# Kernel optimization log

Measured on AMD Instinct MI355X. Metric: run time of the kernel, lower is better.

The kernel has to match this reference:

```python
import jax, jax.numpy as jnp
import numpy as np

B, NQ, NK, H = 4, 2048, 2048, 512
TEMP = 1.0


def setup_inputs() -> dict:
    key = jax.random.key(0)
    ks = jax.random.split(key, 13)
    s = 0.02
    inp = {
        "query_feat": jax.random.normal(ks[0], (B, NQ, H), jnp.float32),
        "key_feat": jax.random.normal(ks[1], (B, NK, H), jnp.float32),
        "qm_uncert": jax.random.normal(ks[2], (B, NQ), jnp.float32),
        "md_uncert": jax.random.normal(ks[3], (B, NK), jnp.float32),
        "Wq": jax.random.normal(ks[4], (H, H), jnp.float32) * s,
        "bq": jnp.zeros((H,), jnp.float32),
        "Wk": jax.random.normal(ks[5], (H, H), jnp.float32) * s,
        "bk": jnp.zeros((H,), jnp.float32),
        "Wv": jax.random.normal(ks[6], (H, H), jnp.float32) * s,
        "bv": jnp.zeros((H,), jnp.float32),
        "Wo": jax.random.normal(ks[7], (H, H), jnp.float32) * s,
        "bo": jnp.zeros((H,), jnp.float32),
        "tau": jnp.float32(1.0),
    }
    return inp


def reference(query_feat, key_feat, qm_uncert, md_uncert,
              Wq, bq, Wk, bk, Wv, bv, Wo, bo, tau):
    h = query_feat.shape[-1]
    Q = query_feat @ Wq.T + bq          # [B,Nq,H]
    K = key_feat @ Wk.T + bk            # [B,Nk,H]
    V = key_feat @ Wv.T + bv            # [B,Nk,H]

    # scaled dot-product logits
    logits = jnp.einsum('bqh,bkh->bqk', Q, K) / jnp.sqrt(jnp.asarray(h, logits_dtype(Q)))

    # uncertainty weight: sigmoid(tau * (qm_i + md_j)), then sanitize (mult mode)
    u = jax.nn.sigmoid(tau * (qm_uncert[:, :, None] + md_uncert[:, None, :]))
    u = jnp.nan_to_num(u, nan=1.0, posinf=1e6, neginf=1e-6)
    u = jnp.clip(u, 1e-6, 1e6)
    row_sum = jnp.sum(jnp.abs(u), axis=-1, keepdims=True)
    u = jnp.where(row_sum <= 1e-12, jnp.asarray(1e-6, u.dtype), u)

    logits = (logits * u) / TEMP

    # rows fully masked to -1e9 get zeroed (no mask here, but kept for faithfulness)
    all_masked = jnp.all(logits == -1e9, axis=-1, keepdims=True)
    logits = jnp.where(all_masked, jnp.zeros_like(logits), logits)

    attn = jax.nn.softmax(logits, axis=-1)  # dropout p=0 -> identity
    att = jnp.einsum('bqk,bkh->bqh', attn, V)
    out = att @ Wo.T + bo
    return out, attn


def logits_dtype(x):
    return x.dtype
```

## Files before the change

### kernel.cpp

```cpp
#include <hip/hip_runtime.h>
#include <stdint.h>

#define DEVI static __device__ __forceinline__

typedef unsigned short u16;
typedef short bf16x8 __attribute__((ext_vector_type(8)));
typedef u16 u16x8 __attribute__((ext_vector_type(8)));
typedef u16 u16x4 __attribute__((ext_vector_type(4)));
typedef float f32x4 __attribute__((ext_vector_type(4)));

DEVI u16 f2bf(float f) {
    uint32_t u = __builtin_bit_cast(uint32_t, f);
    u += 0x7FFFu + ((u >> 16) & 1u);
    return (u16)(u >> 16);
}
DEVI float bf2f(u16 u) { return __builtin_bit_cast(float, (uint32_t)u << 16); }

struct GemmArgs {
    const void* A;
    const void* A2;
    long long aStrideBytes;
    int lda;
    const u16* Bm;
    long long bStrideElts;
    int ldb;
    int K;
    const float* bias; const float* bias2; const float* bias3;
    u16* outB;
    float* outF;
    long long outFStride;
    const float* qm; const float* md; const float* tauPtr; float scale;
    float* partials;
    const float* invsPtr;
    float* invsOut;
    u16* vt;
};

enum { EPI_PROJ3 = 0, EPI_LOGITS = 1, EPI_LOGITSB = 2, EPI_PV = 3, EPI_OUT = 4 };

template <int EPI, int AMODE, int TM, bool U2>
__global__ __launch_bounds__(256, 2) void gemm_bt(GemmArgs p) {
    constexpr int NB = U2 ? 2 : 1;
    constexpr int NF = (TM == 128) ? 4 : 2;
    __shared__ u16 As[NB][TM * 32];
    __shared__ u16 Bs[NB][128 * 32];
    __shared__ float redBuf[2][128];
    __shared__ float sInvLds[128];

    const int tid = threadIdx.x;
    const int lane = tid & 63;
    const int wave = tid >> 6;
    const int g = lane >> 4, lr = lane & 15;
    const int waveRowBase = (TM == 128) ? (wave >> 1) * 64 : 0;
    const int waveColBase = (TM == 128) ? (wave & 1) * 64 : wave * 32;
    const int z = blockIdx.z;
    const int rowBase = blockIdx.x * TM;
    const int colBase = blockIdx.y * 128;

    int batch = z, koff = 0;
    if constexpr (EPI == EPI_PV) { batch = z & 3; koff = (z >> 2) * p.K; }

    const char* Abase;
    const float* bias = p.bias;
    const u16* Bbase;
    if constexpr (EPI == EPI_PROJ3) {
        Abase = (const char*)(z == 0 ? p.A : p.A2);
        Bbase = p.Bm + (size_t)z * 512 * 512;
        bias = (z == 0) ? p.bias : (z == 1 ? p.bias2 : p.bias3);
    } else {
        Abase = (const char*)p.A + (size_t)batch * p.aStrideBytes + (size_t)koff * (AMODE == 1 ? 4 : 2);
        Bbase = p.Bm + (size_t)batch * p.bStrideElts + koff;
    }

    if constexpr (EPI == EPI_PV && AMODE == 0) {
        if (blockIdx.y == 4) {
            if (tid < 128) {
                const float* pp = p.partials + ((size_t)batch * 2048 + rowBase + tid) * 16;
                float s = 0.f;
                #pragma unroll
                for (int t = 0; t < 16; ++t) s += pp[t];
                float inv = 1.0f / s;
                sInvLds[tid] = inv;
                p.invsOut[batch * 2048 + rowBase + tid] = inv;
            }
            __syncthreads();
            const u16* e = (const u16*)Abase + (size_t)rowBase * 2048;
            float* attnOut = p.outF + (size_t)batch * p.outFStride + (size_t)rowBase * 2048 + koff;
            #pragma unroll 4
            for (int it = 0; it < 64; ++it) {
                int cc = it * 256 + tid;
                int row = cc >> 7, colc = (cc & 127) * 8;
                float s = sInvLds[row];
                u16x8 v = *(const u16x8*)(e + (size_t)row * 2048 + colc);
                f32x4 f0, f1;
                f0[0] = bf2f(v[0]) * s; f0[1] = bf2f(v[1]) * s;
                f0[2] = bf2f(v[2]) * s; f0[3] = bf2f(v[3]) * s;
                f1[0] = bf2f(v[4]) * s; f1[1] = bf2f(v[5]) * s;
                f1[2] = bf2f(v[6]) * s; f1[3] = bf2f(v[7]) * s;
                float* dst = attnOut + (size_t)row * 2048 + colc;
                __builtin_nontemporal_store(f0, (f32x4*)dst);
                __builtin_nontemporal_store(f1, (f32x4*)dst + 1);
            }
            return;
        }
    }

    f32x4 acc[4][NF] = {};

    const int arow2 = tid >> 2, kh2 = (tid & 3) << 3;
    const u16* pa0 = nullptr; const u16* pa1 = nullptr; float sInv = 1.0f;
    if constexpr (AMODE == 2) {
        pa0 = (const u16*)p.A + (size_t)(rowBase + arow2) * 512 + kh2;
        pa1 = pa0 + (size_t)8192 * 512;
        sInv = p.invsPtr ? p.invsPtr[rowBase + arow2] : 1.0f;
    }

    const int nk = p.K >> 5;
    for (int kt = 0; kt < nk; kt += NB) {
        const int kb = kt << 5;
        float4 areg[4]; u16x8 a0, a1;
        if constexpr (AMODE == 1) {
            const float* Af = (const float*)Abase;
            const int arow = tid >> 1, kh = (tid & 1) << 4;
            const float* src = Af + (size_t)(rowBase + arow) * p.lda + kb + kh;
            #pragma unroll
            for (int j = 0; j < 4; ++j) areg[j] = ((const float4*)src)[j];
        } else if constexpr (AMODE == 2) {
            a0 = *(const u16x8*)(pa0 + kb);
            a1 = *(const u16x8*)(pa1 + kb);
        }
        __syncthreads();
        if constexpr (AMODE == 1) {
            const int arow = tid >> 1, kh = (tid & 1) << 4;
            u16 tmp[16];
            #pragma unroll
            for (int j = 0; j < 4; ++j) {
                tmp[4 * j + 0] = f2bf(areg[j].x);
                tmp[4 * j + 1] = f2bf(areg[j].y);
                tmp[4 * j + 2] = f2bf(areg[j].z);
                tmp[4 * j + 3] = f2bf(areg[j].w);
            }
            #pragma unroll
            for (int h = 0; h < 2; ++h)
                *(u16x8*)&As[0][arow * 32 + kh + h * 8] = *(u16x8*)&tmp[h * 8];
        } else if constexpr (AMODE == 2) {
            u16 tmp[8];
            #pragma unroll
            for (int j = 0; j < 8; ++j)
                tmp[j] = f2bf((bf2f(a0[j]) + bf2f(a1[j])) * sInv);
            *(u16x8*)&As[0][arow2 * 32 + kh2] = *(u16x8*)tmp;
        } else {
            #pragma unroll
            for (int b = 0; b < NB; ++b)
                #pragma unroll
                for (int i = 0; i < TM / 64; ++i) {
                    int c = i * 256 + tid;
                    const u16* gp = (const u16*)Abase + (size_t)(rowBase + (c >> 2)) * p.lda + kb + b * 32 + (c & 3) * 8;
                    char* lp = (char*)&As[b][0] + (i * 256 + wave * 64) * 16;
                    __builtin_amdgcn_global_load_lds((const __attribute__((address_space(1))) void*)gp,
                                                     (__attribute__((address_space(3))) void*)lp, 16, 0, 0);
                }
        }
        #pragma unroll
        for (int b = 0; b < NB; ++b)
            #pragma unroll
            for (int i = 0; i < 2; ++i) {
                int c = i * 256 + tid;
                const u16* gp = Bbase + (size_t)(colBase + (c >> 2)) * p.ldb + kb + b * 32 + (c & 3) * 8;
                char* lp = (char*)&Bs[b][0] + (i * 256 + wave * 64) * 16;
                __builtin_amdgcn_global_load_lds((const __attribute__((address_space(1))) void*)gp,
                                                 (__attribute__((address_space(3))) void*)lp, 16, 0, 0);
            }
        __syncthreads();

        #pragma unroll
        for (int b = 0; b < NB; ++b) {
            bf16x8 af[4], bfr[NF];
            #pragma unroll
            for (int m = 0; m < 4; ++m)
                af[m] = *(const bf16x8*)&As[b][(waveRowBase + m * 16 + lr) * 32 + g * 8];
            #pragma unroll
            for (int n = 0; n < NF; ++n)
                bfr[n] = *(const bf16x8*)&Bs[b][(waveColBase + n * 16 + lr) * 32 + g * 8];
            #pragma unroll
            for (int m = 0; m < 4; ++m)
                #pragma unroll
                for (int n = 0; n < NF; ++n)
                    acc[m][n] = __builtin_amdgcn_mfma_f32_16x16x32_bf16(af[m], bfr[n], acc[m][n], 0, 0, 0);
        }
    }

    const int rB = rowBase + waveRowBase;
    const int cB = colBase + waveColBase;

    if constexpr (EPI == EPI_PROJ3) {
        if (z < 2) {
            u16* dst = p.outB + (size_t)z * 8192 * 512;
            #pragma unroll
            for (int n = 0; n < NF; ++n) {
                int col = cB + n * 16 + lr;
                float bv = bias[col];
                #pragma unroll
                for (int m = 0; m < 4; ++m) {
                    int r0 = rB + m * 16 + g * 4;
                    #pragma unroll
                    for (int i = 0; i < 4; ++i)
                        dst[(size_t)(r0 + i) * 512 + col] = f2bf(acc[m][n][i] + bv);
                }
            }
        } else {
            #pragma unroll
            for (int n = 0; n < NF; ++n) {
                int col = cB + n * 16 + lr;
                float bv = bias[col];
                #pragma unroll
                for (int m = 0; m < 4; ++m) {
                    int r0 = rB + m * 16 + g * 4;
                    int b = r0 >> 11, k0 = r0 & 2047;
                    u16x4 pk;
                    #pragma unroll
                    for (int i = 0; i < 4; ++i) pk[i] = f2bf(acc[m][n][i] + bv);
                    *(u16x4*)&p.vt[((size_t)b * 512 + col) * 2048 + k0] = pk;
                }
            }
        }
    } else if constexpr (EPI == EPI_LOGITS || EPI == EPI_LOGITSB) {
        const float* qmB = p.qm + z * 2048;
        const float* mdB = p.md + z * 2048;
        const float tau = *p.tauPtr;
        float* outRow = p.outF + (size_t)z * p.outFStride;
        float mdv[NF];
        #pragma unroll
        for (int n = 0; n < NF; ++n) mdv[n] = mdB[cB + n * 16 + lr];
        #pragma unroll
        for (int m = 0; m < 4; ++m) {
            int r0 = rB + m * 16 + g * 4;
            #pragma unroll
            for (int i = 0; i < 4; ++i) {
                int q = r0 + i;
                float qv = qmB[q];
                float rs = 0.f;
                #pragma unroll
                for (int n = 0; n < NF; ++n) {
                    float t = tau * (qv + mdv[n]);
                    float u = 1.0f / (1.0f + __expf(-t));
                    u = fminf(fmaxf(u, 1e-6f), 1e6f);
                    float e = __expf(acc[m][n][i] * p.scale * u);
                    if (EPI == EPI_LOGITSB)
                        p.outB[((size_t)(z * 2048 + q)) * 2048 + cB + n * 16 + lr] = f2bf(e);
                    else
                        outRow[(size_t)q * 2048 + cB + n * 16 + lr] = e;
                    rs += e;
                }
                #pragma unroll
                for (int off = 1; off < 16; off <<= 1) rs += __shfl_xor(rs, off, 64);
                if (lr == 0) redBuf[wave & 1][waveRowBase + m * 16 + g * 4 + i] = rs;
            }
        }
        __syncthreads();
        if (tid < 128) {
            float s = redBuf[0][tid] + redBuf[1][tid];
            int q = rowBase + tid;
            p.partials[((size_t)z * 2048 + q) * 16 + blockIdx.y] = s;
        }
    } else if constexpr (EPI == EPI_PV) {
        const int split = z >> 2;
        u16* dst = p.outB + (size_t)split * 8192 * 512;
        #pragma unroll
        for (int n = 0; n < NF; ++n) {
            int col = cB + n * 16 + lr;
            #pragma unroll
            for (int m = 0; m < 4; ++m) {
                int r0 = rB + m * 16 + g * 4;
                size_t gr = (size_t)batch * 2048 + r0;
                #pragma unroll
                for (int i = 0; i < 4; ++i)
                    dst[(gr + i) * 512 + col] = f2bf(acc[m][n][i]);
            }
        }
    } else {
        #pragma unroll
        for (int n = 0; n < NF; ++n) {
            int col = cB + n * 16 + lr;
            float bv = p.bias[col];
            #pragma unroll
            for (int m = 0; m < 4; ++m) {
                int r0 = rB + m * 16 + g * 4;
                #pragma unroll
                for (int i = 0; i < 4; ++i)
                    __builtin_nontemporal_store(acc[m][n][i] + bv, &p.outF[(size_t)(r0 + i) * 512 + col]);
            }
        }
    }
}

__global__ void cvt_weights(const float* a, const float* b, const float* c, const float* d,
                            u16* dst) {
    const float* src;
    switch (blockIdx.y) {
        case 0: src = a; break;
        case 1: src = b; break;
        case 2: src = c; break;
        default: src = d; break;
    }
    int i = (blockIdx.x * 256 + threadIdx.x) * 4;
    float4 v = *(const float4*)(src + i);
    u16x4 u = { f2bf(v.x), f2bf(v.y), f2bf(v.z), f2bf(v.w) };
    *(u16x4*)(dst + (size_t)blockIdx.y * 512 * 512 + i) = u;
}

__global__ void rowsum_inv(const float* __restrict__ partials, float* __restrict__ invs) {
    int r = blockIdx.x * 256 + threadIdx.x;
    float s = 0.f;
    #pragma unroll
    for (int t = 0; t < 16; ++t) s += partials[r * 16 + t];
    invs[r] = 1.0f / s;
}

__global__ void normalize_attn(float* __restrict__ attn, const float* __restrict__ invs) {
    size_t i4 = (size_t)blockIdx.x * 256 + threadIdx.x;
    int row = (int)(i4 >> 9);
    float s = invs[row];
    float4 v = ((const float4*)attn)[i4];
    v.x *= s; v.y *= s; v.z *= s; v.w *= s;
    ((float4*)attn)[i4] = v;
}

extern "C" void kernel_launch(void* const* d_in, const int* in_sizes, int n_in,
                              void* d_out, int out_size, void* d_ws, size_t ws_size,
                              hipStream_t stream) {
    const float* qf  = (const float*)d_in[0];
    const float* kf  = (const float*)d_in[1];
    const float* qm  = (const float*)d_in[2];
    const float* md  = (const float*)d_in[3];
    const float* Wq  = (const float*)d_in[4];
    const float* bq  = (const float*)d_in[5];
    const float* Wk  = (const float*)d_in[6];
    const float* bk  = (const float*)d_in[7];
    const float* Wv  = (const float*)d_in[8];
    const float* bv  = (const float*)d_in[9];
    const float* Wo  = (const float*)d_in[10];
    const float* bo  = (const float*)d_in[11];
    const float* tau = (const float*)d_in[12];

    float* out  = (float*)d_out;
    float* attn = out + (size_t)4 * 2048 * 512;

    const size_t NV = (size_t)8192 * 512;
    u16* Qb   = (u16*)d_ws;
    u16* Kb   = Qb + NV;
    u16* Vtb  = Kb + NV;
    u16* Wqb  = Vtb + NV;
    u16* Wob  = Wqb + (size_t)3 * 512 * 512;
    float* partials = (float*)(Wqb + (size_t)4 * 512 * 512);
    float* invs = partials + (size_t)8192 * 16;
    u16* attE = (u16*)(invs + 8192);
    size_t need = (size_t)((char*)(attE + (size_t)4 * 2048 * 2048) - (char*)d_ws);
    const bool big = ws_size >= need;

    u16* partialPV = Qb;

    dim3 blk(256);

    cvt_weights<<<dim3(256, 4), blk, 0, stream>>>(Wq, Wk, Wv, Wo, Wqb);

    GemmArgs a = {};
    a.A = qf; a.A2 = kf; a.lda = 512; a.ldb = 512; a.K = 512;
    a.Bm = Wqb;
    a.bias = bq; a.bias2 = bk; a.bias3 = bv;
    a.outB = Qb; a.vt = Vtb;
    gemm_bt<EPI_PROJ3, 1, 128, false><<<dim3(64, 4, 3), blk, 0, stream>>>(a);

    GemmArgs lg = {};
    lg.A = Qb; lg.aStrideBytes = (long long)2048 * 512 * 2; lg.lda = 512;
    lg.Bm = Kb; lg.bStrideElts = (long long)2048 * 512; lg.ldb = 512;
    lg.K = 512;
    lg.qm = qm; lg.md = md; lg.tauPtr = tau;
    lg.scale = 0.04419417382415922f;
    lg.partials = partials;
    if (big) {
        lg.outB = attE;
        gemm_bt<EPI_LOGITSB, 0, 128, true><<<dim3(16, 16, 4), blk, 0, stream>>>(lg);
    } else {
        lg.outF = attn; lg.outFStride = (long long)2048 * 2048;
        gemm_bt<EPI_LOGITS, 0, 128, true><<<dim3(16, 16, 4), blk, 0, stream>>>(lg);
    }

    GemmArgs pv = {};
    pv.Bm = Vtb; pv.bStrideElts = (long long)512 * 2048; pv.ldb = 2048;
    pv.K = 1024; pv.outB = partialPV; pv.lda = 2048;
    pv.partials = partials; pv.invsOut = invs;
    if (big) {
        pv.A = attE; pv.aStrideBytes = (long long)2048 * 2048 * 2;
        pv.outF = attn; pv.outFStride = (long long)2048 * 2048;
        gemm_bt<EPI_PV, 0, 128, true><<<dim3(16, 5, 8), blk, 0, stream>>>(pv);
    } else {
        rowsum_inv<<<dim3(32), blk, 0, stream>>>(partials, invs);
        normalize_attn<<<dim3(16384), blk, 0, stream>>>(attn, invs);
        pv.A = attn; pv.aStrideBytes = (long long)2048 * 2048 * 4;
        gemm_bt<EPI_PV, 1, 128, false><<<dim3(16, 4, 8), blk, 0, stream>>>(pv);
    }

    GemmArgs og = {};
    og.A = partialPV; og.lda = 512;
    og.Bm = Wob; og.ldb = 512;
    og.K = 512; og.bias = bo; og.outF = out;
    og.invsPtr = big ? invs : nullptr;
    gemm_bt<EPI_OUT, 2, 64, false><<<dim3(128, 4, 1), blk, 0, stream>>>(og);
}
```

Measured before the change: 127.6 us.

## Pre-convert query/key features to bf16 and raise GEMM occupancy bound

Converts the fp32 query and key features to bf16 in one fused conversion kernel alongside the weights. The projection GEMM can then use the bf16 A-operand path with double-buffered LDS instead of converting fp32 on the fly. It also raises the launch-bounds minimum blocks per CU from 2 to 4, which pressures register allocation for all GEMM instances. The cost is an extra pass over the 16 MB of inputs and more workspace, and an unused dead kernel (cvt_all) is left behind.

```diff
diff --git a/kernel.cpp b/kernel.cpp
--- a/kernel.cpp
+++ b/kernel.cpp
@@ -39,7 +39,7 @@
 enum { EPI_PROJ3 = 0, EPI_LOGITS = 1, EPI_LOGITSB = 2, EPI_PV = 3, EPI_OUT = 4 };
 
 template <int EPI, int AMODE, int TM, bool U2>
-__global__ __launch_bounds__(256, 2) void gemm_bt(GemmArgs p) {
+__global__ __launch_bounds__(256, 4) void gemm_bt(GemmArgs p) {
     constexpr int NB = U2 ? 2 : 1;
     constexpr int NF = (TM == 128) ? 4 : 2;
     __shared__ u16 As[NB][TM * 32];
@@ -294,19 +294,49 @@
     }
 }
 
-__global__ void cvt_weights(const float* a, const float* b, const float* c, const float* d,
-                            u16* dst) {
-    const float* src;
-    switch (blockIdx.y) {
-        case 0: src = a; break;
-        case 1: src = b; break;
-        case 2: src = c; break;
-        default: src = d; break;
-    }
-    int i = (blockIdx.x * 256 + threadIdx.x) * 4;
-    float4 v = *(const float4*)(src + i);
+__global__ void cvt_all(const float* Wq, const float* Wk, const float* Wv, const float* Wo,
+                        const float* qf, const float* kf,
+                        u16* wdst, u16* qdst, u16* kdst) {
+    const size_t WSZ = (size_t)512 * 512;
+    const size_t FSZ = (size_t)8192 * 512;
+    size_t i = ((size_t)blockIdx.x * 256 + threadIdx.x) * 4;
+    const float* src; u16* dst; size_t off;
+    if (i < 4 * WSZ) {
+        int w = (int)(i / WSZ);
+        src = w == 0 ? Wq : w == 1 ? Wk : w == 2 ? Wv : Wo;
+        off = i - (size_t)w * WSZ;
+        dst = wdst + i;
+    } else if (i < 4 * WSZ + FSZ) {
+        src = qf; off = i - 4 * WSZ; dst = qdst + off;
+    } else {
+        src = kf; off = i - 4 * WSZ - FSZ; dst = kdst + off;
+    }
+    float4 v = *(const float4*)(src + off);
     u16x4 u = { f2bf(v.x), f2bf(v.y), f2bf(v.z), f2bf(v.w) };
-    *(u16x4*)(dst + (size_t)blockIdx.y * 512 * 512 + i) = u;
+    *(u16x4*)(dst + off - (off - (dst == wdst + i ? 0 : 0))) = u;
+}
+
+__global__ void cvt_all2(const float* Wq, const float* Wk, const float* Wv, const float* Wo,
+                         const float* qf, const float* kf,
+                         u16* wdst, u16* qdst, u16* kdst) {
+    const size_t WSZ = (size_t)512 * 512;
+    const size_t FSZ = (size_t)8192 * 512;
+    size_t i = ((size_t)blockIdx.x * 256 + threadIdx.x) * 4;
+    const float* src; u16* dstp;
+    if (i < 4 * WSZ) {
+        int w = (int)(i / WSZ);
+        src = (w == 0 ? Wq : w == 1 ? Wk : w == 2 ? Wv : Wo) + (i - (size_t)w * WSZ);
+        dstp = wdst + i;
+    } else if (i < 4 * WSZ + FSZ) {
+        size_t off = i - 4 * WSZ;
+        src = qf + off; dstp = qdst + off;
+    } else {
+        size_t off = i - 4 * WSZ - FSZ;
+        src = kf + off; dstp = kdst + off;
+    }
+    float4 v = *(const float4*)src;
+    u16x4 u = { f2bf(v.x), f2bf(v.y), f2bf(v.z), f2bf(v.w) };
+    *(u16x4*)dstp = u;
 }
 
 __global__ void rowsum_inv(const float* __restrict__ partials, float* __restrict__ invs) {
@@ -355,21 +385,28 @@
     float* partials = (float*)(Wqb + (size_t)4 * 512 * 512);
     float* invs = partials + (size_t)8192 * 16;
     u16* attE = (u16*)(invs + 8192);
-    size_t need = (size_t)((char*)(attE + (size_t)4 * 2048 * 2048) - (char*)d_ws);
+    u16* qfB  = attE + (size_t)4 * 2048 * 2048;
+    u16* kfB  = qfB + NV;
+    size_t need = (size_t)((char*)(kfB + NV) - (char*)d_ws);
     const bool big = ws_size >= need;
 
     u16* partialPV = Qb;
 
     dim3 blk(256);
 
-    cvt_weights<<<dim3(256, 4), blk, 0, stream>>>(Wq, Wk, Wv, Wo, Wqb);
-
     GemmArgs a = {};
-    a.A = qf; a.A2 = kf; a.lda = 512; a.ldb = 512; a.K = 512;
-    a.Bm = Wqb;
+    a.lda = 512; a.ldb = 512; a.K = 512;
     a.bias = bq; a.bias2 = bk; a.bias3 = bv;
     a.outB = Qb; a.vt = Vtb;
-    gemm_bt<EPI_PROJ3, 1, 128, false><<<dim3(64, 4, 3), blk, 0, stream>>>(a);
+    if (big) {
+        cvt_all2<<<dim3(9216), blk, 0, stream>>>(Wq, Wk, Wv, Wo, qf, kf, Wqb, qfB, kfB);
+        a.A = qfB; a.A2 = kfB; a.Bm = Wqb;
+        gemm_bt<EPI_PROJ3, 0, 128, true><<<dim3(64, 4, 3), blk, 0, stream>>>(a);
+    } else {
+        cvt_all2<<<dim3(1024), blk, 0, stream>>>(Wq, Wk, Wv, Wo, qf, kf, Wqb, nullptr, nullptr);
+        a.A = qf; a.A2 = kf; a.Bm = Wqb;
+        gemm_bt<EPI_PROJ3, 1, 128, false><<<dim3(64, 4, 3), blk, 0, stream>>>(a);
+    }
 
     GemmArgs lg = {};
     lg.A = Qb; lg.aStrideBytes = (long long)2048 * 512 * 2; lg.lda = 512;
```

After: 126.0 us. Within noise of the previous version (-1.3%).
